# Kernel tuning notes

Measured on AMD Instinct MI355X. Metric: run time of the kernel, lower is better.

## Reference

```python
import jax, jax.numpy as jnp
import numpy as np

D_MODEL = 1024
NUM_HEADS = 16
DEPTH = D_MODEL // NUM_HEADS


def setup_inputs() -> dict:
    key = jax.random.key(0)
    ks = jax.random.split(key, 9)
    B, S = 2, 2048
    scale = 1.0 / np.sqrt(D_MODEL)
    x = jax.random.normal(ks[0], (B, S, D_MODEL), dtype=jnp.float32)
    wq = jax.random.normal(ks[1], (D_MODEL, D_MODEL), dtype=jnp.float32) * scale
    wk = jax.random.normal(ks[2], (D_MODEL, D_MODEL), dtype=jnp.float32) * scale
    wv = jax.random.normal(ks[3], (D_MODEL, D_MODEL), dtype=jnp.float32) * scale
    wo = jax.random.normal(ks[4], (D_MODEL, D_MODEL), dtype=jnp.float32) * scale
    bq = jnp.zeros((D_MODEL,), dtype=jnp.float32)
    bk = jnp.zeros((D_MODEL,), dtype=jnp.float32)
    bv = jnp.zeros((D_MODEL,), dtype=jnp.float32)
    bo = jnp.zeros((D_MODEL,), dtype=jnp.float32)
    return {"x": x, "wq": wq, "bq": bq, "wk": wk, "bk": bk,
            "wv": wv, "bv": bv, "wo": wo, "bo": bo}


def _split_heads(t):
    # [B, S, D] -> [B, H, S, depth]
    B, S, _ = t.shape
    return t.reshape(B, S, NUM_HEADS, DEPTH).transpose(0, 2, 1, 3)


def reference(x, wq, bq, wk, bk, wv, bv, wo, bo):
    q = _split_heads(x @ wq + bq)
    k = _split_heads(x @ wk + bk)
    v = _split_heads(x @ wv + bv)
    # scaled dot-product attention with materialized [B,H,S,S] scores
    logits = jnp.einsum("bhqd,bhkd->bhqk", q, k) / jnp.sqrt(
        jnp.asarray(DEPTH, dtype=x.dtype))
    attn = jax.nn.softmax(logits, axis=-1)
    out = jnp.einsum("bhqk,bhkd->bhqd", attn, v)
    B, _, S, _ = out.shape
    concat = out.transpose(0, 2, 1, 3).reshape(B, S, D_MODEL)
    return concat @ wo + bo
```

## Files before the change

### kernel.cpp

```cpp
#include <hip/hip_runtime.h>
#include <hip/hip_bf16.h>
#include <stdint.h>

typedef unsigned short u16;
typedef __attribute__((ext_vector_type(8))) short short8;
typedef __attribute__((ext_vector_type(4))) short s4v;
typedef __attribute__((ext_vector_type(4))) float f32x4;

__device__ __forceinline__ float bf2f(u16 u) {
    union { uint32_t u; float f; } v; v.u = ((uint32_t)u) << 16; return v.f;
}
__device__ __forceinline__ u16 f2bf(float f) {
    union { float f; uint32_t u; } v; v.f = f;
    uint32_t r = (v.u + 0x7fffu + ((v.u >> 16) & 1u)) >> 16;
    return (u16)r;
}
__device__ __forceinline__ uint32_t pkbf(float a, float b) {
    union { __hip_bfloat162 h; uint32_t w; } u;
    u.h = __float22bfloat162_rn(float2{a, b});
    return u.w;
}
__device__ __forceinline__ void store_out(u16* p, float v) { *p = f2bf(v); }
__device__ __forceinline__ void store_out(float* p, float v) { *p = v; }

__device__ __forceinline__ void async_ld16(const u16* g, u16* l) {
    __builtin_amdgcn_global_load_lds(
        (const __attribute__((address_space(1))) void*)g,
        (__attribute__((address_space(3))) void*)l, 16, 0, 0);
}

__global__ void prep(const float* __restrict__ x,
                     const float* __restrict__ w0, const float* __restrict__ w1,
                     const float* __restrict__ w2,
                     u16* __restrict__ xb, u16* __restrict__ wT) {
    const int z = blockIdx.z;
    __shared__ u16 tile[32][33];
    if (z >= 3) {
        int blk = (z - 3) * 1024 + blockIdx.y * 32 + blockIdx.x;
        int tid = threadIdx.y * 32 + threadIdx.x;
        int i = (blk * 256 + tid) * 8;
        float4 a = *(const float4*)(x + i);
        float4 b = *(const float4*)(x + i + 4);
        union { uint32_t w[4]; uint4 v; } o;
        o.w[0] = pkbf(a.x, a.y); o.w[1] = pkbf(a.z, a.w);
        o.w[2] = pkbf(b.x, b.y); o.w[3] = pkbf(b.z, b.w);
        *(uint4*)(xb + i) = o.v;
        return;
    }
    const float* in = (z == 0) ? w0 : (z == 1) ? w1 : w2;
    u16* o = wT + (size_t)z * 1024 * 1024;
    int xx = blockIdx.x * 32 + threadIdx.x;
    int y0 = blockIdx.y * 32;
#pragma unroll
    for (int j = threadIdx.y; j < 32; j += 8)
        tile[j][threadIdx.x] = f2bf(in[(size_t)(y0 + j) * 1024 + xx]);
    __syncthreads();
    int ox = blockIdx.y * 32 + threadIdx.x;
    int oy0 = blockIdx.x * 32;
#pragma unroll
    for (int j = threadIdx.y; j < 32; j += 8)
        o[(size_t)(oy0 + j) * 1024 + ox] = tile[threadIdx.x][j];
}

__global__ void transpose1(const float* __restrict__ w, u16* __restrict__ out) {
    __shared__ u16 tile[32][33];
    int x = blockIdx.x * 32 + threadIdx.x;
    int y0 = blockIdx.y * 32;
#pragma unroll
    for (int j = threadIdx.y; j < 32; j += 8)
        tile[j][threadIdx.x] = f2bf(w[(size_t)(y0 + j) * 1024 + x]);
    __syncthreads();
    int ox = blockIdx.y * 32 + threadIdx.x;
    int oy0 = blockIdx.x * 32;
#pragma unroll
    for (int j = threadIdx.y; j < 32; j += 8)
        out[(size_t)(oy0 + j) * 1024 + ox] = tile[threadIdx.x][j];
}

#define GBM 128
#define GBN 128
#define GBK 32

template <typename OutT>
__global__ __launch_bounds__(256) void gemm_bt(
    const u16* __restrict__ A, int lda,
    const u16* __restrict__ BT, int ldb,
    const float* __restrict__ bias0, const float* __restrict__ bias1,
    const float* __restrict__ bias2,
    OutT* __restrict__ C, int ldc, int K) {
    __shared__ __align__(16) u16 As[2][GBM * GBK];
    __shared__ __align__(16) u16 Bs[2][GBN * GBK];

    const int tid = threadIdx.x;
    const int wave = tid >> 6, lane = tid & 63;
    const int quad = lane >> 4, l16 = lane & 15;
    const int wr = wave >> 1, wc = wave & 1;
    const int m0 = blockIdx.y * GBM, n0 = blockIdx.x * GBN;

    const int seg = n0 >> 10;
    const float* bsel = (seg == 0) ? bias0 : (seg == 1) ? bias1 : bias2;

    f32x4 acc[4][4] = {};

    const int srow = tid >> 2;
    const int scol = (tid & 3) * 8;
    const u16* Ag0 = A + (size_t)(m0 + srow) * lda + scol;
    const u16* Ag1 = Ag0 + (size_t)64 * lda;
    const u16* Bg0 = BT + (size_t)(n0 + srow) * ldb + scol;
    const u16* Bg1 = Bg0 + (size_t)64 * ldb;
    const int woff = wave << 9;

    async_ld16(Ag0, As[0] + woff);
    async_ld16(Ag1, As[0] + woff + 64 * GBK);
    async_ld16(Bg0, Bs[0] + woff);
    async_ld16(Bg1, Bs[0] + woff + 64 * GBK);

    int cur = 0;
    for (int kb = 0; kb < K; kb += GBK) {
        __syncthreads();

        if (kb + GBK < K) {
            const int nxt = cur ^ 1;
            async_ld16(Ag0 + kb + GBK, As[nxt] + woff);
            async_ld16(Ag1 + kb + GBK, As[nxt] + woff + 64 * GBK);
            async_ld16(Bg0 + kb + GBK, Bs[nxt] + woff);
            async_ld16(Bg1 + kb + GBK, Bs[nxt] + woff + 64 * GBK);
        }

        short8 af[4], bf[4];
#pragma unroll
        for (int mt = 0; mt < 4; mt++)
            af[mt] = *(const short8*)(As[cur] + (wr * 64 + mt * 16 + l16) * GBK + quad * 8);
#pragma unroll
        for (int nt = 0; nt < 4; nt++)
            bf[nt] = *(const short8*)(Bs[cur] + (wc * 64 + nt * 16 + l16) * GBK + quad * 8);
#pragma unroll
        for (int mt = 0; mt < 4; mt++)
#pragma unroll
            for (int nt = 0; nt < 4; nt++)
                acc[mt][nt] = __builtin_amdgcn_mfma_f32_16x16x32_bf16(
                    af[mt], bf[nt], acc[mt][nt], 0, 0, 0);
        cur ^= 1;
    }

#pragma unroll
    for (int nt = 0; nt < 4; nt++) {
        int col = n0 + wc * 64 + nt * 16 + l16;
        float bv = bsel[col & 1023];
#pragma unroll
        for (int mt = 0; mt < 4; mt++) {
            int row = m0 + wr * 64 + mt * 16 + quad * 4;
#pragma unroll
            for (int r = 0; r < 4; r++)
                store_out(&C[(size_t)(row + r) * ldc + col], acc[mt][nt][r] + bv);
        }
    }
}

__global__ __launch_bounds__(256) void gemm_bt64(
    const u16* __restrict__ A, int lda,
    const u16* __restrict__ BT, int ldb,
    const float* __restrict__ bias,
    float* __restrict__ C, int ldc, int K) {
    __shared__ __align__(16) u16 As[2][64 * GBK];
    __shared__ __align__(16) u16 Bs[2][128 * GBK];

    const int tid = threadIdx.x;
    const int wave = tid >> 6, lane = tid & 63;
    const int quad = lane >> 4, l16 = lane & 15;
    const int m0 = blockIdx.y * 64, n0 = blockIdx.x * 128;

    f32x4 acc[4][2] = {};

    const int srow = tid >> 2;
    const int scol = (tid & 3) * 8;
    const u16* Ag0 = A + (size_t)(m0 + srow) * lda + scol;
    const u16* Bg0 = BT + (size_t)(n0 + srow) * ldb + scol;
    const u16* Bg1 = Bg0 + (size_t)64 * ldb;
    const int woff = wave << 9;

    async_ld16(Ag0, As[0] + woff);
    async_ld16(Bg0, Bs[0] + woff);
    async_ld16(Bg1, Bs[0] + woff + 64 * GBK);

    int cur = 0;
    for (int kb = 0; kb < K; kb += GBK) {
        __syncthreads();

        if (kb + GBK < K) {
            const int nxt = cur ^ 1;
            async_ld16(Ag0 + kb + GBK, As[nxt] + woff);
            async_ld16(Bg0 + kb + GBK, Bs[nxt] + woff);
            async_ld16(Bg1 + kb + GBK, Bs[nxt] + woff + 64 * GBK);
        }

        short8 af[4], bf[2];
#pragma unroll
        for (int mt = 0; mt < 4; mt++)
            af[mt] = *(const short8*)(As[cur] + (mt * 16 + l16) * GBK + quad * 8);
#pragma unroll
        for (int nt = 0; nt < 2; nt++)
            bf[nt] = *(const short8*)(Bs[cur] + (wave * 32 + nt * 16 + l16) * GBK + quad * 8);
#pragma unroll
        for (int mt = 0; mt < 4; mt++)
#pragma unroll
            for (int nt = 0; nt < 2; nt++)
                acc[mt][nt] = __builtin_amdgcn_mfma_f32_16x16x32_bf16(
                    af[mt], bf[nt], acc[mt][nt], 0, 0, 0);
        cur ^= 1;
    }

#pragma unroll
    for (int nt = 0; nt < 2; nt++) {
        int col = n0 + wave * 32 + nt * 16 + l16;
        float bv = bias[col & 1023];
#pragma unroll
        for (int mt = 0; mt < 4; mt++) {
            int row = m0 + mt * 16 + quad * 4;
#pragma unroll
            for (int r = 0; r < 4; r++)
                C[(size_t)(row + r) * ldc + col] = acc[mt][nt][r] + bv;
        }
    }
}

#define SEQ 2048
#define BQT 128
#define BKV 128
#define LDK 72
#define LDKV 136

__global__ __launch_bounds__(256) void attn(u16* __restrict__ QKV) {
    __shared__ __align__(16) u16 Ks[BKV * LDK];
    __shared__ __align__(16) u16 Vs[64 * LDKV];

    const int tid = threadIdx.x;
    const int wave = tid >> 6, lane = tid & 63;
    const int quad = lane >> 4, l16 = lane & 15;
    const int h = blockIdx.y, bb = blockIdx.z;
    const int q0 = blockIdx.x * BQT;
    const size_t tok0 = (size_t)bb * SEQ;

    const u16* Qb = QKV + tok0 * 3072 + h * 64;
    const u16* Kb = QKV + tok0 * 3072 + 1024 + h * 64;
    const u16* Vb = QKV + tok0 * 3072 + 2048 + h * 64;

    const float cs = 0.18033688011112042f;

    int qr[2];
    qr[0] = q0 + wave * 16 + l16;
    qr[1] = qr[0] + 64;
    short8 aq[2][2];
#pragma unroll
    for (int s = 0; s < 2; s++) {
        union { short8 v; u16 u[8]; uint32_t w[4]; } qa, qb;
        qa.v = *(const short8*)(Qb + (size_t)qr[s] * 3072 + quad * 8);
        qb.v = *(const short8*)(Qb + (size_t)qr[s] * 3072 + 32 + quad * 8);
#pragma unroll
        for (int j = 0; j < 4; j++) {
            qa.w[j] = pkbf(bf2f(qa.u[2 * j]) * cs, bf2f(qa.u[2 * j + 1]) * cs);
            qb.w[j] = pkbf(bf2f(qb.u[2 * j]) * cs, bf2f(qb.u[2 * j + 1]) * cs);
        }
        aq[s][0] = qa.v; aq[s][1] = qb.v;
    }

    f32x4 o[2][4] = {};
    f32x4 o_l[2] = {};

    const short8 vone = {16256, 16256, 16256, 16256,
                         16256, 16256, 16256, 16256};

    const int srow = tid >> 2;
    const int scc = (tid & 3) * 16;
    const int pr = tid & 63;
    const int dg = wave;

    const u16* kg = Kb + (size_t)srow * 3072 + scc;
    const u16* vg = Vb + (size_t)(2 * pr) * 3072 + dg * 16;

    const int kvb = 2 * pr;
    const int kvp = (kvb & 96) | (((kvb >> 2) & 3) << 3) |
                    (((kvb >> 4) & 1) << 2) | (kvb & 3);

    uint4 k0r = *(const uint4*)(kg);
    uint4 k1r = *(const uint4*)(kg + 8);
    uint4 k2r = *(const uint4*)(kg + (size_t)64 * 3072);
    uint4 k3r = *(const uint4*)(kg + (size_t)64 * 3072 + 8);
    uint4 va0 = *(const uint4*)(vg);
    uint4 va1 = *(const uint4*)(vg + 8);
    uint4 vb0 = *(const uint4*)(vg + 3072);
    uint4 vb1 = *(const uint4*)(vg + 3072 + 8);

    for (int j0 = 0; j0 < SEQ; j0 += BKV) {
        *(uint4*)(Ks + srow * LDK + scc) = k0r;
        *(uint4*)(Ks + srow * LDK + scc + 8) = k1r;
        *(uint4*)(Ks + (srow + 64) * LDK + scc) = k2r;
        *(uint4*)(Ks + (srow + 64) * LDK + scc + 8) = k3r;
        {
            union { uint4 v[2]; u16 u[16]; } a, b;
            a.v[0] = va0; a.v[1] = va1; b.v[0] = vb0; b.v[1] = vb1;
#pragma unroll
            for (int j = 0; j < 16; j++) {
                uint32_t w = (uint32_t)a.u[j] | ((uint32_t)b.u[j] << 16);
                *(uint32_t*)(Vs + (dg * 16 + j) * LDKV + kvp) = w;
            }
        }
        __syncthreads();

        if (j0 + BKV < SEQ) {
            size_t off = (size_t)(j0 + BKV) * 3072;
            k0r = *(const uint4*)(kg + off);
            k1r = *(const uint4*)(kg + off + 8);
            k2r = *(const uint4*)(kg + off + (size_t)64 * 3072);
            k3r = *(const uint4*)(kg + off + (size_t)64 * 3072 + 8);
            va0 = *(const uint4*)(vg + off);
            va1 = *(const uint4*)(vg + off + 8);
            vb0 = *(const uint4*)(vg + off + 3072);
            vb1 = *(const uint4*)(vg + off + 3072 + 8);
        }

        f32x4 st[2][8];
#pragma unroll
        for (int kkt = 0; kkt < 8; kkt++) {
            f32x4 s0 = {}, s1 = {};
#pragma unroll
            for (int k2 = 0; k2 < 2; k2++) {
                short8 ak = *(const short8*)(Ks + (kkt * 16 + l16) * LDK + k2 * 32 + quad * 8);
                s0 = __builtin_amdgcn_mfma_f32_16x16x32_bf16(ak, aq[0][k2], s0, 0, 0, 0);
                s1 = __builtin_amdgcn_mfma_f32_16x16x32_bf16(ak, aq[1][k2], s1, 0, 0, 0);
            }
            st[0][kkt] = s0; st[1][kkt] = s1;
        }

#pragma unroll
        for (int s = 0; s < 2; s++)
#pragma unroll
            for (int kkt = 0; kkt < 8; kkt++)
#pragma unroll
                for (int r = 0; r < 4; r++)
                    st[s][kkt][r] = __builtin_amdgcn_exp2f(st[s][kkt][r]);

#pragma unroll
        for (int tt = 0; tt < 4; tt++) {
            union { uint32_t w[4]; short8 v; } bp0, bp1;
            bp0.w[0] = pkbf(st[0][2 * tt][0], st[0][2 * tt][1]);
            bp0.w[1] = pkbf(st[0][2 * tt][2], st[0][2 * tt][3]);
            bp0.w[2] = pkbf(st[0][2 * tt + 1][0], st[0][2 * tt + 1][1]);
            bp0.w[3] = pkbf(st[0][2 * tt + 1][2], st[0][2 * tt + 1][3]);
            bp1.w[0] = pkbf(st[1][2 * tt][0], st[1][2 * tt][1]);
            bp1.w[1] = pkbf(st[1][2 * tt][2], st[1][2 * tt][3]);
            bp1.w[2] = pkbf(st[1][2 * tt + 1][0], st[1][2 * tt + 1][1]);
            bp1.w[3] = pkbf(st[1][2 * tt + 1][2], st[1][2 * tt + 1][3]);

            o_l[0] = __builtin_amdgcn_mfma_f32_16x16x32_bf16(vone, bp0.v, o_l[0], 0, 0, 0);
            o_l[1] = __builtin_amdgcn_mfma_f32_16x16x32_bf16(vone, bp1.v, o_l[1], 0, 0, 0);
#pragma unroll
            for (int dt = 0; dt < 4; dt++) {
                short8 av = *(const short8*)(Vs + (dt * 16 + l16) * LDKV +
                                             tt * 32 + quad * 8);
                o[0][dt] = __builtin_amdgcn_mfma_f32_16x16x32_bf16(av, bp0.v, o[0][dt], 0, 0, 0);
                o[1][dt] = __builtin_amdgcn_mfma_f32_16x16x32_bf16(av, bp1.v, o[1][dt], 0, 0, 0);
            }
        }

        __syncthreads();
    }

#pragma unroll
    for (int s = 0; s < 2; s++) {
        const float inv_l = 1.0f / o_l[s][0];
        u16* orow = QKV + (tok0 + qr[s]) * 3072 + h * 64;
#pragma unroll
        for (int dt = 0; dt < 4; dt++) {
            uint32_t w0 = pkbf(o[s][dt][0] * inv_l, o[s][dt][1] * inv_l);
            uint32_t w1 = pkbf(o[s][dt][2] * inv_l, o[s][dt][3] * inv_l);
            uint2 w = {w0, w1};
            *(uint2*)(orow + dt * 16 + quad * 4) = w;
        }
    }
}

extern "C" void kernel_launch(void* const* d_in, const int* in_sizes, int n_in,
                              void* d_out, int out_size, void* d_ws, size_t ws_size,
                              hipStream_t stream) {
    const float* x  = (const float*)d_in[0];
    const float* wq = (const float*)d_in[1];
    const float* bq = (const float*)d_in[2];
    const float* wk = (const float*)d_in[3];
    const float* bk = (const float*)d_in[4];
    const float* wv = (const float*)d_in[5];
    const float* bv = (const float*)d_in[6];
    const float* wo = (const float*)d_in[7];
    const float* bo = (const float*)d_in[8];
    (void)in_sizes; (void)n_in; (void)out_size; (void)ws_size;

    u16* QKV = (u16*)d_ws;
    u16* wT  = QKV + (size_t)4096 * 3072;
    u16* xb  = wT + (size_t)3 * 1024 * 1024;
    u16* woT = xb;

    prep<<<dim3(32, 32, 5), dim3(32, 8), 0, stream>>>(x, wq, wk, wv, xb, wT);
    gemm_bt<u16><<<dim3(24, 32), 256, 0, stream>>>(xb, 1024, wT, 1024, bq, bk, bv,
                                                   QKV, 3072, 1024);
    transpose1<<<dim3(32, 32), dim3(32, 8), 0, stream>>>(wo, woT);
    attn<<<dim3(16, 16, 2), 256, 0, stream>>>(QKV);
    gemm_bt64<<<dim3(8, 64), 256, 0, stream>>>(QKV, 3072, woT, 1024, bo,
                                               (float*)d_out, 1024, 1024);
}
```

Before: 203.7 us.

## Remap GEMM tiles per XCD and async double-buffer swizzled K tiles in attention

Both GEMM kernels now remap workgroup IDs so that blocks dispatched to the same XCD cover contiguous tile regions, aiming for better L2 reuse of A and B panels. The remap only applies to the specific grid shapes. In attention, K tiles are loaded with async global-to-LDS copies into a double-buffered, XOR-swizzled LDS layout instead of staging through registers into a padded array. This removes register staging and bank-conflict padding, but doubles K LDS usage and depends on the async wait being handled correctly in the loop.

```diff
diff --git a/kernel.cpp b/kernel.cpp
--- a/kernel.cpp
+++ b/kernel.cpp
@@ -4,7 +4,6 @@
 
 typedef unsigned short u16;
 typedef __attribute__((ext_vector_type(8))) short short8;
-typedef __attribute__((ext_vector_type(4))) short s4v;
 typedef __attribute__((ext_vector_type(4))) float f32x4;
 
 __device__ __forceinline__ float bf2f(u16 u) {
@@ -95,7 +94,15 @@
     const int wave = tid >> 6, lane = tid & 63;
     const int quad = lane >> 4, l16 = lane & 15;
     const int wr = wave >> 1, wc = wave & 1;
-    const int m0 = blockIdx.y * GBM, n0 = blockIdx.x * GBN;
+
+    int bx = blockIdx.x, by = blockIdx.y;
+    if (gridDim.x == 24 && gridDim.y == 32) {
+        const int wgid = blockIdx.x + blockIdx.y * 24;
+        const int xcd = wgid & 7, t = wgid >> 3;
+        bx = (xcd & 1) * 12 + t % 12;
+        by = (xcd >> 1) * 8 + t / 12;
+    }
+    const int m0 = by * GBM, n0 = bx * GBN;
 
     const int seg = n0 >> 10;
     const float* bsel = (seg == 0) ? bias0 : (seg == 1) ? bias1 : bias2;
@@ -168,7 +175,15 @@
     const int tid = threadIdx.x;
     const int wave = tid >> 6, lane = tid & 63;
     const int quad = lane >> 4, l16 = lane & 15;
-    const int m0 = blockIdx.y * 64, n0 = blockIdx.x * 128;
+
+    int bx = blockIdx.x, by = blockIdx.y;
+    if (gridDim.x == 8 && gridDim.y == 64) {
+        const int wgid = blockIdx.x + blockIdx.y * 8;
+        const int xcd = wgid & 7, t = wgid >> 3;
+        bx = t & 7;
+        by = (xcd << 3) + (t >> 3);
+    }
+    const int m0 = by * 64, n0 = bx * 128;
 
     f32x4 acc[4][2] = {};
 
@@ -227,11 +242,10 @@
 #define SEQ 2048
 #define BQT 128
 #define BKV 128
-#define LDK 72
 #define LDKV 136
 
 __global__ __launch_bounds__(256) void attn(u16* __restrict__ QKV) {
-    __shared__ __align__(16) u16 Ks[BKV * LDK];
+    __shared__ __align__(16) u16 Ks[2][BKV * 64];
     __shared__ __align__(16) u16 Vs[64 * LDKV];
 
     const int tid = threadIdx.x;
@@ -270,32 +284,29 @@
     const short8 vone = {16256, 16256, 16256, 16256,
                          16256, 16256, 16256, 16256};
 
-    const int srow = tid >> 2;
-    const int scc = (tid & 3) * 16;
+    const int krow = tid >> 3;
+    const int kcs = (tid & 7) ^ (krow & 7);
+    const u16* kgs = Kb + (size_t)krow * 3072 + kcs * 8;
+    const int ksw0 = ((quad) ^ (l16 & 7)) * 8;
+    const int ksw1 = ((quad + 4) ^ (l16 & 7)) * 8;
+
     const int pr = tid & 63;
     const int dg = wave;
-
-    const u16* kg = Kb + (size_t)srow * 3072 + scc;
     const u16* vg = Vb + (size_t)(2 * pr) * 3072 + dg * 16;
-
     const int kvb = 2 * pr;
     const int kvp = (kvb & 96) | (((kvb >> 2) & 3) << 3) |
                     (((kvb >> 4) & 1) << 2) | (kvb & 3);
 
-    uint4 k0r = *(const uint4*)(kg);
-    uint4 k1r = *(const uint4*)(kg + 8);
-    uint4 k2r = *(const uint4*)(kg + (size_t)64 * 3072);
-    uint4 k3r = *(const uint4*)(kg + (size_t)64 * 3072 + 8);
+#pragma unroll
+    for (int i = 0; i < 4; i++)
+        async_ld16(kgs + (size_t)(i * 32) * 3072, &Ks[0][i * 2048 + wave * 512]);
     uint4 va0 = *(const uint4*)(vg);
     uint4 va1 = *(const uint4*)(vg + 8);
     uint4 vb0 = *(const uint4*)(vg + 3072);
     uint4 vb1 = *(const uint4*)(vg + 3072 + 8);
 
+    int cur = 0;
     for (int j0 = 0; j0 < SEQ; j0 += BKV) {
-        *(uint4*)(Ks + srow * LDK + scc) = k0r;
-        *(uint4*)(Ks + srow * LDK + scc + 8) = k1r;
-        *(uint4*)(Ks + (srow + 64) * LDK + scc) = k2r;
-        *(uint4*)(Ks + (srow + 64) * LDK + scc + 8) = k3r;
         {
             union { uint4 v[2]; u16 u[16]; } a, b;
             a.v[0] = va0; a.v[1] = va1; b.v[0] = vb0; b.v[1] = vb1;
@@ -308,11 +319,12 @@
         __syncthreads();
 
         if (j0 + BKV < SEQ) {
-            size_t off = (size_t)(j0 + BKV) * 3072;
-            k0r = *(const uint4*)(kg + off);
-            k1r = *(const uint4*)(kg + off + 8);
-            k2r = *(const uint4*)(kg + off + (size_t)64 * 3072);
-            k3r = *(const uint4*)(kg + off + (size_t)64 * 3072 + 8);
+            const size_t off = (size_t)(j0 + BKV) * 3072;
+            const int nxt = cur ^ 1;
+#pragma unroll
+            for (int i = 0; i < 4; i++)
+                async_ld16(kgs + off + (size_t)(i * 32) * 3072,
+                           &Ks[nxt][i * 2048 + wave * 512]);
             va0 = *(const uint4*)(vg + off);
             va1 = *(const uint4*)(vg + off + 8);
             vb0 = *(const uint4*)(vg + off + 3072);
@@ -322,13 +334,14 @@
         f32x4 st[2][8];
 #pragma unroll
         for (int kkt = 0; kkt < 8; kkt++) {
+            const u16* kr = &Ks[cur][(kkt * 16 + l16) * 64];
+            short8 ak0 = *(const short8*)(kr + ksw0);
+            short8 ak1 = *(const short8*)(kr + ksw1);
             f32x4 s0 = {}, s1 = {};
-#pragma unroll
-            for (int k2 = 0; k2 < 2; k2++) {
-                short8 ak = *(const short8*)(Ks + (kkt * 16 + l16) * LDK + k2 * 32 + quad * 8);
-                s0 = __builtin_amdgcn_mfma_f32_16x16x32_bf16(ak, aq[0][k2], s0, 0, 0, 0);
-                s1 = __builtin_amdgcn_mfma_f32_16x16x32_bf16(ak, aq[1][k2], s1, 0, 0, 0);
-            }
+            s0 = __builtin_amdgcn_mfma_f32_16x16x32_bf16(ak0, aq[0][0], s0, 0, 0, 0);
+            s1 = __builtin_amdgcn_mfma_f32_16x16x32_bf16(ak0, aq[1][0], s1, 0, 0, 0);
+            s0 = __builtin_amdgcn_mfma_f32_16x16x32_bf16(ak1, aq[0][1], s0, 0, 0, 0);
+            s1 = __builtin_amdgcn_mfma_f32_16x16x32_bf16(ak1, aq[1][1], s1, 0, 0, 0);
             st[0][kkt] = s0; st[1][kkt] = s1;
         }
 
@@ -364,6 +377,7 @@
         }
 
         __syncthreads();
+        cur ^= 1;
     }
 
 #pragma unroll
```

Result: no change. 207.0 us (+1.6%).
